# Performance work log

Hardware: AMD Instinct MI355X
Metric: run time of the kernel (lower is better)

The kernel has to match this reference:

```python
import jax, jax.numpy as jnp
import numpy as np

D_MODEL = 1024
EXPAND = 2
D_INNER = D_MODEL * EXPAND
KERNEL = 4
EPS = 1e-5


def setup_inputs() -> dict:
    key = jax.random.key(0)
    ks = jax.random.split(key, 8)
    B, L = 2, 4096
    x = jax.random.normal(ks[0], (B, L, D_MODEL), dtype=jnp.float32)
    norm_w = jnp.ones((D_MODEL,), jnp.float32)
    norm_b = jnp.zeros((D_MODEL,), jnp.float32)
    # torch Linear weight layout [out, in]
    in_proj_w = jax.random.normal(ks[1], (2 * D_INNER, D_MODEL), jnp.float32) / np.sqrt(D_MODEL)
    # depthwise Conv1d weight [d_inner, 1, K]
    conv_w = jax.random.normal(ks[2], (D_INNER, 1, KERNEL), jnp.float32) / np.sqrt(KERNEL)
    conv_b = jax.random.normal(ks[3], (D_INNER,), jnp.float32) * 0.02
    gate_w = jax.random.normal(ks[4], (D_INNER, D_INNER), jnp.float32) / np.sqrt(D_INNER)
    gate_b = jnp.zeros((D_INNER,), jnp.float32)
    out_proj_w = jax.random.normal(ks[5], (D_MODEL, D_INNER), jnp.float32) / np.sqrt(D_INNER)
    return {"x": x, "norm_w": norm_w, "norm_b": norm_b, "in_proj_w": in_proj_w,
            "conv_w": conv_w, "conv_b": conv_b, "gate_w": gate_w, "gate_b": gate_b,
            "out_proj_w": out_proj_w}


def _layernorm(x, w, b):
    mu = jnp.mean(x, axis=-1, keepdims=True)
    var = jnp.var(x, axis=-1, keepdims=True)
    return (x - mu) * jax.lax.rsqrt(var + EPS) * w + b


def _glru(x, norm_w, norm_b, in_proj_w, conv_w, conv_b, gate_w, gate_b, out_proj_w):
    B, L, D = x.shape
    residual = x
    xn = _layernorm(x, norm_w, norm_b)
    xz = jnp.einsum('bld,ed->ble', xn, in_proj_w)  # [B,L,2*d_inner]
    x_inner, z = jnp.split(xz, 2, axis=-1)
    # causal depthwise conv: torch pads 3 both sides then slices [:L] == left-pad 3
    lhs = jnp.transpose(x_inner, (0, 2, 1))  # [B, C, L]
    conv = jax.lax.conv_general_dilated(
        lhs, conv_w, window_strides=(1,), padding=[(KERNEL - 1, 0)],
        feature_group_count=D_INNER,
        dimension_numbers=('NCH', 'OIH', 'NCH'))
    x_conv = jnp.transpose(conv, (0, 2, 1)) + conv_b  # [B, L, C]
    x_conv = jax.nn.silu(x_conv)
    a = jax.nn.sigmoid(jnp.einsum('blc,ec->ble', x_conv, gate_w) + gate_b)
    b = (1.0 - a) * x_conv
    # h_t = a_t * h_{t-1} + b_t, h_0 prior = 0 -> parallel associative scan
    def combine(e1, e2):
        a1, b1 = e1
        a2, b2 = e2
        return a1 * a2, a2 * b1 + b2
    _, y = jax.lax.associative_scan(combine, (a, b), axis=1)
    y = y * jax.nn.silu(z)
    return residual + jnp.einsum('blc,dc->bld', y, out_proj_w)


def reference(x, norm_w, norm_b, in_proj_w, conv_w, conv_b, gate_w, gate_b, out_proj_w):
    return _glru(x, norm_w, norm_b, in_proj_w, conv_w, conv_b, gate_w, gate_b, out_proj_w)
```

## Files before the change

### kernel.cpp

```cpp
#include <hip/hip_runtime.h>
#include <cstdint>

#define D_MODEL 1024
#define D_INNER 2048
#define LSEQ    4096
#define BATCH   2
#define M_ROWS  (BATCH * LSEQ)
#define CHUNK   128
#define NCHUNK  (LSEQ / CHUNK)

typedef unsigned short u16;
typedef __bf16 bf16x8 __attribute__((ext_vector_type(8)));
typedef float f32x4 __attribute__((ext_vector_type(4)));
typedef u16 u16x4 __attribute__((ext_vector_type(4)));

__device__ __forceinline__ u16 f2bf(float f) {
  union { float f; unsigned u; } x; x.f = f;
  unsigned u = x.u;
  unsigned r = (u + 0x7FFFu + ((u >> 16) & 1u)) >> 16;
  return (u16)r;
}
__device__ __forceinline__ float bf2f(u16 h) {
  union { unsigned u; float f; } x; x.u = ((unsigned)h) << 16;
  return x.f;
}
__device__ __forceinline__ float sigmoidf_(float v) { return 1.0f / (1.0f + expf(-v)); }
__device__ __forceinline__ float siluf_(float v)    { return v / (1.0f + expf(-v)); }

__device__ __forceinline__ void gl_lds16(const void* g, void* l) {
  __builtin_amdgcn_global_load_lds(
      (const __attribute__((address_space(1))) void*)g,
      (__attribute__((address_space(3))) void*)l, 16, 0, 0);
}

#define SBAR()   asm volatile("s_barrier" ::: "memory")
#define WAITV0() asm volatile("s_waitcnt vmcnt(0)" ::: "memory")
#define WAITV2() asm volatile("s_waitcnt vmcnt(2)" ::: "memory")
#define WAITV8() asm volatile("s_waitcnt vmcnt(8)" ::: "memory")
#define WAITL0() do { asm volatile("s_waitcnt lgkmcnt(0)" ::: "memory"); __builtin_amdgcn_sched_barrier(0); } while (0)

__global__ void __launch_bounds__(256)
cast_bf16_kernel(const float* __restrict__ in, u16* __restrict__ out, int n4) {
  int i = blockIdx.x * 256 + threadIdx.x;
  if (i < n4) {
    float4 v = ((const float4*)in)[i];
    u16x4 o;
    o.x = f2bf(v.x); o.y = f2bf(v.y); o.z = f2bf(v.z); o.w = f2bf(v.w);
    ((u16x4*)out)[i] = o;
  }
}

__global__ void __launch_bounds__(256)
ln_kernel(const float* __restrict__ x, const float* __restrict__ w,
          const float* __restrict__ b, u16* __restrict__ xn) {
  const int row = blockIdx.x;
  const int t = threadIdx.x;
  const float4 v = ((const float4*)(x + (size_t)row * D_MODEL))[t];
  float s  = v.x + v.y + v.z + v.w;
  float ss = v.x * v.x + v.y * v.y + v.z * v.z + v.w * v.w;
#pragma unroll
  for (int o = 32; o > 0; o >>= 1) {
    s  += __shfl_xor(s, o);
    ss += __shfl_xor(ss, o);
  }
  __shared__ float red[8];
  const int wid = t >> 6, lane = t & 63;
  if (lane == 0) { red[wid] = s; red[4 + wid] = ss; }
  __syncthreads();
  s  = red[0] + red[1] + red[2] + red[3];
  ss = red[4] + red[5] + red[6] + red[7];
  const float mu  = s * (1.0f / D_MODEL);
  const float var = ss * (1.0f / D_MODEL) - mu * mu;
  const float rs  = rsqrtf(var + 1e-5f);
  const float4 wv = ((const float4*)w)[t];
  const float4 bv = ((const float4*)b)[t];
  u16x4 o4;
  o4.x = f2bf((v.x - mu) * rs * wv.x + bv.x);
  o4.y = f2bf((v.y - mu) * rs * wv.y + bv.y);
  o4.z = f2bf((v.z - mu) * rs * wv.z + bv.z);
  o4.w = f2bf((v.w - mu) * rs * wv.w + bv.w);
  ((u16x4*)(xn + (size_t)row * D_MODEL))[t] = o4;
}

#define MFMA_BF16 __builtin_amdgcn_mfma_f32_16x16x32_bf16

template<int EPI>
__global__ void __launch_bounds__(512, 2)
gemm256(const u16* __restrict__ A, const u16* __restrict__ Bm,
        int M, int N, int K,
        const float* __restrict__ ef, float* __restrict__ of,
        u16* __restrict__ ob0, u16* __restrict__ ob1) {
  __shared__ __align__(1024) char lds[131072];
  const int tid  = threadIdx.x;
  const int wid  = tid >> 6, lane = tid & 63;
  const int nbx  = N >> 8;
  const int nwg  = nbx * (M >> 8);
  const int bid  = blockIdx.x;
  const int cpx  = nwg >> 3;
  const int swz  = (bid & 7) * cpx + (bid >> 3);
  const int bx   = swz % nbx, by = swz / nbx;
  const size_t m0 = (size_t)by << 8, n0 = (size_t)bx << 8;

  const int wr = wid >> 2, wc = wid & 3;
  const size_t rb = (size_t)K * 2;
  const size_t rj = (size_t)64 * rb;

  const int srow  = lane >> 3;
  const int sslot = ((lane & 7) ^ srow) << 4;
  const char* gA = (const char*)A  + (m0 + (size_t)(wid * 8 + srow)) * rb + sslot;
  const char* gB = (const char*)Bm + (n0 + (size_t)(wid * 8 + srow)) * rb + sslot;
  const int sdst = wid * 1024;

  const int q    = lane >> 4;
  const int r15  = lane & 15;
  const int cswz0 = (q * 16)      ^ ((lane & 7) << 4);
  const int cswz1 = (64 + q * 16) ^ ((lane & 7) << 4);
  const int paoff = (wr * 128 + r15) * 128;
  const int pboff = (wc * 64  + r15) * 128;

  f32x4 acc[8][4] = {};
  const int nk = K >> 6;

  {
    const char* a = gA; const char* b = gB;
#pragma unroll
    for (int i = 0; i < 4; ++i) {
      gl_lds16(a, lds + sdst + i * 8192);
      gl_lds16(b, lds + 65536 + sdst + i * 8192);
      a += rj; b += rj;
    }
  }
  WAITV0();
  SBAR();

  size_t kb = 128;
  for (int t = 0; t < nk; ++t) {
    const int cur = t & 1;
    const char* At = lds + cur * 32768;
    const char* Bt = lds + 65536 + cur * 32768;
    char* An = lds + (cur ^ 1) * 32768;
    char* Bn = lds + 65536 + (cur ^ 1) * 32768;
    const bool pf = (t + 1 < nk);

    bf16x8 af[4][2], b0[2][2], b1[2][2];

    if (pf) {
      gl_lds16(gA + kb,          An + sdst);
      gl_lds16(gA + kb + 2 * rj, An + sdst + 16384);
      gl_lds16(gB + kb,          Bn + sdst);
      gl_lds16(gB + kb + rj,     Bn + sdst + 8192);
      gl_lds16(gB + kb + 2 * rj, Bn + sdst + 16384);
      gl_lds16(gB + kb + 3 * rj, Bn + sdst + 24576);
      gl_lds16(gA + kb + rj,     An + sdst + 8192);
      gl_lds16(gA + kb + 3 * rj, An + sdst + 24576);
    }
#pragma unroll
    for (int mi = 0; mi < 4; ++mi) {
      af[mi][0] = *(const bf16x8*)(At + paoff + mi * 2048 + cswz0);
      af[mi][1] = *(const bf16x8*)(At + paoff + mi * 2048 + cswz1);
    }
#pragma unroll
    for (int ni = 0; ni < 2; ++ni) {
      b0[ni][0] = *(const bf16x8*)(Bt + pboff + ni * 2048 + cswz0);
      b0[ni][1] = *(const bf16x8*)(Bt + pboff + ni * 2048 + cswz1);
    }
    SBAR();
    WAITL0();
    __builtin_amdgcn_s_setprio(1);
#pragma unroll
    for (int mi = 0; mi < 4; ++mi)
#pragma unroll
      for (int ni = 0; ni < 2; ++ni) {
        acc[mi][ni] = MFMA_BF16(af[mi][0], b0[ni][0], acc[mi][ni], 0, 0, 0);
        acc[mi][ni] = MFMA_BF16(af[mi][1], b0[ni][1], acc[mi][ni], 0, 0, 0);
      }
    __builtin_amdgcn_s_setprio(0);
    SBAR();

#pragma unroll
    for (int ni = 0; ni < 2; ++ni) {
      b1[ni][0] = *(const bf16x8*)(Bt + pboff + (ni + 2) * 2048 + cswz0);
      b1[ni][1] = *(const bf16x8*)(Bt + pboff + (ni + 2) * 2048 + cswz1);
    }
    SBAR();
    WAITL0();
    __builtin_amdgcn_s_setprio(1);
#pragma unroll
    for (int mi = 0; mi < 4; ++mi)
#pragma unroll
      for (int ni = 0; ni < 2; ++ni) {
        acc[mi][ni + 2] = MFMA_BF16(af[mi][0], b1[ni][0], acc[mi][ni + 2], 0, 0, 0);
        acc[mi][ni + 2] = MFMA_BF16(af[mi][1], b1[ni][1], acc[mi][ni + 2], 0, 0, 0);
      }
    __builtin_amdgcn_s_setprio(0);
    if (pf) { WAITV8(); } else { WAITV0(); }
    SBAR();

#pragma unroll
    for (int mi = 0; mi < 4; ++mi) {
      af[mi][0] = *(const bf16x8*)(At + paoff + (mi + 4) * 2048 + cswz0);
      af[mi][1] = *(const bf16x8*)(At + paoff + (mi + 4) * 2048 + cswz1);
    }
    SBAR();
    WAITL0();
    __builtin_amdgcn_s_setprio(1);
#pragma unroll
    for (int mi = 0; mi < 4; ++mi)
#pragma unroll
      for (int ni = 0; ni < 2; ++ni) {
        acc[mi + 4][ni] = MFMA_BF16(af[mi][0], b0[ni][0], acc[mi + 4][ni], 0, 0, 0);
        acc[mi + 4][ni] = MFMA_BF16(af[mi][1], b0[ni][1], acc[mi + 4][ni], 0, 0, 0);
      }
    __builtin_amdgcn_s_setprio(0);
    SBAR();

    __builtin_amdgcn_s_setprio(1);
#pragma unroll
    for (int mi = 0; mi < 4; ++mi)
#pragma unroll
      for (int ni = 0; ni < 2; ++ni) {
        acc[mi + 4][ni + 2] = MFMA_BF16(af[mi][0], b1[ni][0], acc[mi + 4][ni + 2], 0, 0, 0);
        acc[mi + 4][ni + 2] = MFMA_BF16(af[mi][1], b1[ni][1], acc[mi + 4][ni + 2], 0, 0, 0);
      }
    __builtin_amdgcn_s_setprio(0);
    if (pf) { WAITV2(); }
    SBAR();
    kb += 128;
  }

  const int c0 = lane & 15;
  const int r0 = (lane >> 4) << 2;
#pragma unroll
  for (int mi = 0; mi < 8; ++mi) {
#pragma unroll
    for (int ni = 0; ni < 4; ++ni) {
#pragma unroll
      for (int rg = 0; rg < 4; ++rg) {
        const size_t row = m0 + (size_t)(wr * 128 + mi * 16 + r0 + rg);
        const size_t col = n0 + (size_t)(wc * 64 + ni * 16 + c0);
        const float v = acc[mi][ni][rg];
        if (EPI == 0) {
          if (col < (size_t)D_INNER) ob0[row * D_INNER + col] = f2bf(v);
          else                       ob1[row * D_INNER + (col - D_INNER)] = f2bf(siluf_(v));
        } else if (EPI == 1) {
          ob0[row * (size_t)N + col] = f2bf(v);
        } else {
          of[row * (size_t)N + col] = v + ef[row * (size_t)N + col];
        }
      }
    }
  }
}

__global__ void __launch_bounds__(256)
conv_silu_kernel(const u16* __restrict__ xin, const float* __restrict__ cw,
                 const float* __restrict__ cb, u16* __restrict__ xc) {
  const int c   = blockIdx.x * 256 + threadIdx.x;
  const int l0  = blockIdx.y * 8;
  const int bat = blockIdx.z;
  const size_t base = ((size_t)bat * LSEQ) * D_INNER + c;
  const float w0 = cw[c * 4 + 0], w1 = cw[c * 4 + 1], w2 = cw[c * 4 + 2], w3 = cw[c * 4 + 3];
  const float bb = cb[c];
  float v[11];
#pragma unroll
  for (int i = 0; i < 11; ++i) {
    const int l = l0 - 3 + i;
    v[i] = (l >= 0) ? bf2f(xin[base + (size_t)l * D_INNER]) : 0.0f;
  }
#pragma unroll
  for (int r = 0; r < 8; ++r) {
    const float acc = bb + w0 * v[r] + w1 * v[r + 1] + w2 * v[r + 2] + w3 * v[r + 3];
    xc[base + (size_t)(l0 + r) * D_INNER] = f2bf(siluf_(acc));
  }
}

__global__ void __launch_bounds__(256)
scan_a_kernel(const u16* __restrict__ g, const u16* __restrict__ xc,
              const float* __restrict__ gbias,
              float* __restrict__ cA, float* __restrict__ cB) {
  const int c   = (blockIdx.x * 256 + threadIdx.x) * 2;
  const int ch  = blockIdx.y;
  const int bat = blockIdx.z;
  const float bb0 = gbias[c], bb1 = gbias[c + 1];
  size_t idx = ((size_t)bat * LSEQ + (size_t)ch * CHUNK) * D_INNER + c;
  float pA0 = 1.0f, hB0 = 0.0f, pA1 = 1.0f, hB1 = 0.0f;
  for (int t = 0; t < CHUNK; ++t) {
    const ushort2 gg = *(const ushort2*)(g + idx);
    const ushort2 xx = *(const ushort2*)(xc + idx);
    const float a0 = sigmoidf_(bf2f(gg.x) + bb0);
    const float a1 = sigmoidf_(bf2f(gg.y) + bb1);
    pA0 *= a0; hB0 = a0 * hB0 + (1.0f - a0) * bf2f(xx.x);
    pA1 *= a1; hB1 = a1 * hB1 + (1.0f - a1) * bf2f(xx.y);
    idx += D_INNER;
  }
  const size_t o = ((size_t)bat * NCHUNK + ch) * D_INNER + c;
  *(float2*)(cA + o) = make_float2(pA0, pA1);
  *(float2*)(cB + o) = make_float2(hB0, hB1);
}

__global__ void __launch_bounds__(256)
scan_b_kernel(const float* __restrict__ cA, const float* __restrict__ cB,
              float* __restrict__ carry) {
  const int tid = blockIdx.x * 256 + threadIdx.x;
  const int bat = tid >> 11;
  const int c   = tid & (D_INNER - 1);
  float h = 0.0f;
  const size_t base = (size_t)bat * NCHUNK * D_INNER + c;
  for (int i = 0; i < NCHUNK; ++i) {
    const size_t o = base + (size_t)i * D_INNER;
    carry[o] = h;
    h = cA[o] * h + cB[o];
  }
}

__global__ void __launch_bounds__(256)
scan_c_kernel(const u16* __restrict__ g, const u16* __restrict__ xc,
              const u16* __restrict__ sz, const float* __restrict__ gbias,
              const float* __restrict__ carry, u16* __restrict__ yg) {
  const int c   = (blockIdx.x * 256 + threadIdx.x) * 2;
  const int ch  = blockIdx.y;
  const int bat = blockIdx.z;
  const float bb0 = gbias[c], bb1 = gbias[c + 1];
  const float2 h2 = *(const float2*)(carry + ((size_t)bat * NCHUNK + ch) * D_INNER + c);
  float h0 = h2.x, h1 = h2.y;
  size_t idx = ((size_t)bat * LSEQ + (size_t)ch * CHUNK) * D_INNER + c;
  for (int t = 0; t < CHUNK; ++t) {
    const ushort2 gg = *(const ushort2*)(g + idx);
    const ushort2 xx = *(const ushort2*)(xc + idx);
    const ushort2 zz = *(const ushort2*)(sz + idx);
    const float a0 = sigmoidf_(bf2f(gg.x) + bb0);
    const float a1 = sigmoidf_(bf2f(gg.y) + bb1);
    h0 = a0 * h0 + (1.0f - a0) * bf2f(xx.x);
    h1 = a1 * h1 + (1.0f - a1) * bf2f(xx.y);
    ushort2 o2;
    o2.x = f2bf(h0 * bf2f(zz.x));
    o2.y = f2bf(h1 * bf2f(zz.y));
    *(ushort2*)(yg + idx) = o2;
    idx += D_INNER;
  }
}

extern "C" void kernel_launch(void* const* d_in, const int* in_sizes, int n_in,
                              void* d_out, int out_size, void* d_ws, size_t ws_size,
                              hipStream_t stream) {
  const float* x         = (const float*)d_in[0];
  const float* norm_w    = (const float*)d_in[1];
  const float* norm_b    = (const float*)d_in[2];
  const float* in_proj_w = (const float*)d_in[3];
  const float* conv_w    = (const float*)d_in[4];
  const float* conv_b    = (const float*)d_in[5];
  const float* gate_w    = (const float*)d_in[6];
  const float* gate_b    = (const float*)d_in[7];
  const float* out_proj_w= (const float*)d_in[8];
  float* out = (float*)d_out;

  char* p = (char*)d_ws;
  u16* xn      = (u16*)p; p += (size_t)M_ROWS * D_MODEL * 2;
  u16* w_in    = (u16*)p; p += (size_t)2 * D_INNER * D_MODEL * 2;
  u16* w_gate  = (u16*)p; p += (size_t)D_INNER * D_INNER * 2;
  u16* w_out   = (u16*)p; p += (size_t)D_MODEL * D_INNER * 2;
  u16* x_inner = (u16*)p; p += (size_t)M_ROWS * D_INNER * 2;
  u16* szb     = (u16*)p; p += (size_t)M_ROWS * D_INNER * 2;
  u16* xconv   = (u16*)p; p += (size_t)M_ROWS * D_INNER * 2;
  u16* gbuf    = (u16*)p; p += (size_t)M_ROWS * D_INNER * 2;
  u16* yg      = (u16*)p; p += (size_t)M_ROWS * D_INNER * 2;
  float* cA    = (float*)p; p += (size_t)BATCH * NCHUNK * D_INNER * 4;
  float* cB    = (float*)p; p += (size_t)BATCH * NCHUNK * D_INNER * 4;
  float* carry = (float*)p; p += (size_t)BATCH * NCHUNK * D_INNER * 4;
  if ((size_t)(p - (char*)d_ws) > ws_size) return;

  cast_bf16_kernel<<<dim3(2 * D_INNER * D_MODEL / 4 / 256), 256, 0, stream>>>(in_proj_w, w_in, 2 * D_INNER * D_MODEL / 4);
  cast_bf16_kernel<<<dim3(D_INNER * D_INNER / 4 / 256), 256, 0, stream>>>(gate_w, w_gate, D_INNER * D_INNER / 4);
  cast_bf16_kernel<<<dim3(D_MODEL * D_INNER / 4 / 256), 256, 0, stream>>>(out_proj_w, w_out, D_MODEL * D_INNER / 4);

  ln_kernel<<<dim3(M_ROWS), 256, 0, stream>>>(x, norm_w, norm_b, xn);

  gemm256<0><<<dim3((M_ROWS / 256) * (2 * D_INNER / 256)), 512, 0, stream>>>(
      xn, w_in, M_ROWS, 2 * D_INNER, D_MODEL, nullptr, nullptr, x_inner, szb);

  conv_silu_kernel<<<dim3(D_INNER / 256, LSEQ / 8, BATCH), 256, 0, stream>>>(x_inner, conv_w, conv_b, xconv);

  gemm256<1><<<dim3((M_ROWS / 256) * (D_INNER / 256)), 512, 0, stream>>>(
      xconv, w_gate, M_ROWS, D_INNER, D_INNER, nullptr, nullptr, gbuf, nullptr);

  scan_a_kernel<<<dim3(D_INNER / 512, NCHUNK, BATCH), 256, 0, stream>>>(gbuf, xconv, gate_b, cA, cB);
  scan_b_kernel<<<dim3(BATCH * D_INNER / 256), 256, 0, stream>>>(cA, cB, carry);
  scan_c_kernel<<<dim3(D_INNER / 512, NCHUNK, BATCH), 256, 0, stream>>>(gbuf, xconv, szb, gate_b, carry, yg);

  gemm256<2><<<dim3((M_ROWS / 256) * (D_MODEL / 256)), 512, 0, stream>>>(
      yg, w_out, M_ROWS, D_MODEL, D_INNER, x, out, nullptr, nullptr);
}
```

Measured before the change: 368.0 us.

## Software-pipeline GEMM LDS fragment loads across k-iterations and drop occupancy hint

Restructures the gemm256 main loop so the A-low and B0 fragments for the next k-tile are read from LDS at the end of the current iteration, overlapping LDS reads with MFMA work. Several barriers and explicit lgkmcnt waits are removed, and the global-to-LDS prefetch is split into two phases with new vmcnt wait points. The launch-bounds occupancy hint of 2 blocks is dropped, giving the compiler more registers for the extra live fragments at the cost of possible occupancy. The epilogue branch on column is hoisted to a per-block flag.

```diff
diff --git a/kernel.cpp b/kernel.cpp
--- a/kernel.cpp
+++ b/kernel.cpp
@@ -35,9 +35,7 @@
 
 #define SBAR()   asm volatile("s_barrier" ::: "memory")
 #define WAITV0() asm volatile("s_waitcnt vmcnt(0)" ::: "memory")
-#define WAITV2() asm volatile("s_waitcnt vmcnt(2)" ::: "memory")
-#define WAITV8() asm volatile("s_waitcnt vmcnt(8)" ::: "memory")
-#define WAITL0() do { asm volatile("s_waitcnt lgkmcnt(0)" ::: "memory"); __builtin_amdgcn_sched_barrier(0); } while (0)
+#define WAITV6() asm volatile("s_waitcnt vmcnt(6)" ::: "memory")
 
 __global__ void __launch_bounds__(256)
 cast_bf16_kernel(const float* __restrict__ in, u16* __restrict__ out, int n4) {
@@ -85,7 +83,7 @@
 #define MFMA_BF16 __builtin_amdgcn_mfma_f32_16x16x32_bf16
 
 template<int EPI>
-__global__ void __launch_bounds__(512, 2)
+__global__ void __launch_bounds__(512)
 gemm256(const u16* __restrict__ A, const u16* __restrict__ Bm,
         int M, int N, int K,
         const float* __restrict__ ef, float* __restrict__ of,
@@ -119,6 +117,7 @@
   const int pboff = (wc * 64  + r15) * 128;
 
   f32x4 acc[8][4] = {};
+  bf16x8 afL[4][2], afH[4][2], b0r[2][2], b1r[2][2];
   const int nk = K >> 6;
 
   {
@@ -132,6 +131,20 @@
   }
   WAITV0();
   SBAR();
+  {
+    const char* At = lds;
+    const char* Bt = lds + 65536;
+#pragma unroll
+    for (int mi = 0; mi < 4; ++mi) {
+      afL[mi][0] = *(const bf16x8*)(At + paoff + mi * 2048 + cswz0);
+      afL[mi][1] = *(const bf16x8*)(At + paoff + mi * 2048 + cswz1);
+    }
+#pragma unroll
+    for (int ni = 0; ni < 2; ++ni) {
+      b0r[ni][0] = *(const bf16x8*)(Bt + pboff + ni * 2048 + cswz0);
+      b0r[ni][1] = *(const bf16x8*)(Bt + pboff + ni * 2048 + cswz1);
+    }
+  }
 
   size_t kb = 128;
   for (int t = 0; t < nk; ++t) {
@@ -142,8 +155,6 @@
     char* Bn = lds + 65536 + (cur ^ 1) * 32768;
     const bool pf = (t + 1 < nk);
 
-    bf16x8 af[4][2], b0[2][2], b1[2][2];
-
     if (pf) {
       gl_lds16(gA + kb,          An + sdst);
       gl_lds16(gA + kb + 2 * rj, An + sdst + 16384);
@@ -151,85 +162,82 @@
       gl_lds16(gB + kb + rj,     Bn + sdst + 8192);
       gl_lds16(gB + kb + 2 * rj, Bn + sdst + 16384);
       gl_lds16(gB + kb + 3 * rj, Bn + sdst + 24576);
+    }
+#pragma unroll
+    for (int ni = 0; ni < 2; ++ni) {
+      b1r[ni][0] = *(const bf16x8*)(Bt + pboff + (ni + 2) * 2048 + cswz0);
+      b1r[ni][1] = *(const bf16x8*)(Bt + pboff + (ni + 2) * 2048 + cswz1);
+    }
+    __builtin_amdgcn_s_setprio(1);
+#pragma unroll
+    for (int mi = 0; mi < 4; ++mi)
+#pragma unroll
+      for (int ni = 0; ni < 2; ++ni) {
+        acc[mi][ni] = MFMA_BF16(afL[mi][0], b0r[ni][0], acc[mi][ni], 0, 0, 0);
+        acc[mi][ni] = MFMA_BF16(afL[mi][1], b0r[ni][1], acc[mi][ni], 0, 0, 0);
+      }
+    __builtin_amdgcn_s_setprio(0);
+    if (pf) { WAITV6(); } else { WAITV0(); }
+    SBAR();
+
+#pragma unroll
+    for (int mi = 0; mi < 4; ++mi) {
+      afH[mi][0] = *(const bf16x8*)(At + paoff + (mi + 4) * 2048 + cswz0);
+      afH[mi][1] = *(const bf16x8*)(At + paoff + (mi + 4) * 2048 + cswz1);
+    }
+    __builtin_amdgcn_s_setprio(1);
+#pragma unroll
+    for (int mi = 0; mi < 4; ++mi)
+#pragma unroll
+      for (int ni = 0; ni < 2; ++ni) {
+        acc[mi][ni + 2] = MFMA_BF16(afL[mi][0], b1r[ni][0], acc[mi][ni + 2], 0, 0, 0);
+        acc[mi][ni + 2] = MFMA_BF16(afL[mi][1], b1r[ni][1], acc[mi][ni + 2], 0, 0, 0);
+      }
+    __builtin_amdgcn_s_setprio(0);
+    SBAR();
+
+    __builtin_amdgcn_s_setprio(1);
+#pragma unroll
+    for (int mi = 0; mi < 4; ++mi)
+#pragma unroll
+      for (int ni = 0; ni < 2; ++ni) {
+        acc[mi + 4][ni] = MFMA_BF16(afH[mi][0], b0r[ni][0], acc[mi + 4][ni], 0, 0, 0);
+        acc[mi + 4][ni] = MFMA_BF16(afH[mi][1], b0r[ni][1], acc[mi + 4][ni], 0, 0, 0);
+      }
+    __builtin_amdgcn_s_setprio(0);
+    WAITV0();
+    SBAR();
+
+    if (pf) {
       gl_lds16(gA + kb + rj,     An + sdst + 8192);
       gl_lds16(gA + kb + 3 * rj, An + sdst + 24576);
-    }
-#pragma unroll
-    for (int mi = 0; mi < 4; ++mi) {
-      af[mi][0] = *(const bf16x8*)(At + paoff + mi * 2048 + cswz0);
-      af[mi][1] = *(const bf16x8*)(At + paoff + mi * 2048 + cswz1);
-    }
-#pragma unroll
-    for (int ni = 0; ni < 2; ++ni) {
-      b0[ni][0] = *(const bf16x8*)(Bt + pboff + ni * 2048 + cswz0);
-      b0[ni][1] = *(const bf16x8*)(Bt + pboff + ni * 2048 + cswz1);
-    }
-    SBAR();
-    WAITL0();
+#pragma unroll
+      for (int mi = 0; mi < 4; ++mi) {
+        afL[mi][0] = *(const bf16x8*)(An + paoff + mi * 2048 + cswz0);
+        afL[mi][1] = *(const bf16x8*)(An + paoff + mi * 2048 + cswz1);
+      }
+#pragma unroll
+      for (int ni = 0; ni < 2; ++ni) {
+        b0r[ni][0] = *(const bf16x8*)(Bn + pboff + ni * 2048 + cswz0);
+        b0r[ni][1] = *(const bf16x8*)(Bn + pboff + ni * 2048 + cswz1);
+      }
+    }
     __builtin_amdgcn_s_setprio(1);
 #pragma unroll
     for (int mi = 0; mi < 4; ++mi)
 #pragma unroll
       for (int ni = 0; ni < 2; ++ni) {
-        acc[mi][ni] = MFMA_BF16(af[mi][0], b0[ni][0], acc[mi][ni], 0, 0, 0);
-        acc[mi][ni] = MFMA_BF16(af[mi][1], b0[ni][1], acc[mi][ni], 0, 0, 0);
+        acc[mi + 4][ni + 2] = MFMA_BF16(afH[mi][0], b1r[ni][0], acc[mi + 4][ni + 2], 0, 0, 0);
+        acc[mi + 4][ni + 2] = MFMA_BF16(afH[mi][1], b1r[ni][1], acc[mi + 4][ni + 2], 0, 0, 0);
       }
     __builtin_amdgcn_s_setprio(0);
     SBAR();
-
-#pragma unroll
-    for (int ni = 0; ni < 2; ++ni) {
-      b1[ni][0] = *(const bf16x8*)(Bt + pboff + (ni + 2) * 2048 + cswz0);
-      b1[ni][1] = *(const bf16x8*)(Bt + pboff + (ni + 2) * 2048 + cswz1);
-    }
-    SBAR();
-    WAITL0();
-    __builtin_amdgcn_s_setprio(1);
-#pragma unroll
-    for (int mi = 0; mi < 4; ++mi)
-#pragma unroll
-      for (int ni = 0; ni < 2; ++ni) {
-        acc[mi][ni + 2] = MFMA_BF16(af[mi][0], b1[ni][0], acc[mi][ni + 2], 0, 0, 0);
-        acc[mi][ni + 2] = MFMA_BF16(af[mi][1], b1[ni][1], acc[mi][ni + 2], 0, 0, 0);
-      }
-    __builtin_amdgcn_s_setprio(0);
-    if (pf) { WAITV8(); } else { WAITV0(); }
-    SBAR();
-
-#pragma unroll
-    for (int mi = 0; mi < 4; ++mi) {
-      af[mi][0] = *(const bf16x8*)(At + paoff + (mi + 4) * 2048 + cswz0);
-      af[mi][1] = *(const bf16x8*)(At + paoff + (mi + 4) * 2048 + cswz1);
-    }
-    SBAR();
-    WAITL0();
-    __builtin_amdgcn_s_setprio(1);
-#pragma unroll
-    for (int mi = 0; mi < 4; ++mi)
-#pragma unroll
-      for (int ni = 0; ni < 2; ++ni) {
-        acc[mi + 4][ni] = MFMA_BF16(af[mi][0], b0[ni][0], acc[mi + 4][ni], 0, 0, 0);
-        acc[mi + 4][ni] = MFMA_BF16(af[mi][1], b0[ni][1], acc[mi + 4][ni], 0, 0, 0);
-      }
-    __builtin_amdgcn_s_setprio(0);
-    SBAR();
-
-    __builtin_amdgcn_s_setprio(1);
-#pragma unroll
-    for (int mi = 0; mi < 4; ++mi)
-#pragma unroll
-      for (int ni = 0; ni < 2; ++ni) {
-        acc[mi + 4][ni + 2] = MFMA_BF16(af[mi][0], b1[ni][0], acc[mi + 4][ni + 2], 0, 0, 0);
-        acc[mi + 4][ni + 2] = MFMA_BF16(af[mi][1], b1[ni][1], acc[mi + 4][ni + 2], 0, 0, 0);
-      }
-    __builtin_amdgcn_s_setprio(0);
-    if (pf) { WAITV2(); }
-    SBAR();
     kb += 128;
   }
 
   const int c0 = lane & 15;
   const int r0 = (lane >> 4) << 2;
+  const bool isz = (EPI == 0) && (n0 >= (size_t)D_INNER);
 #pragma unroll
   for (int mi = 0; mi < 8; ++mi) {
 #pragma unroll
@@ -240,8 +248,8 @@
         const size_t col = n0 + (size_t)(wc * 64 + ni * 16 + c0);
         const float v = acc[mi][ni][rg];
         if (EPI == 0) {
-          if (col < (size_t)D_INNER) ob0[row * D_INNER + col] = f2bf(v);
-          else                       ob1[row * D_INNER + (col - D_INNER)] = f2bf(siluf_(v));
+          if (!isz) ob0[row * D_INNER + col] = f2bf(v);
+          else      ob1[row * D_INNER + (col - D_INNER)] = f2bf(siluf_(v));
         } else if (EPI == 1) {
           ob0[row * (size_t)N + col] = f2bf(v);
         } else {
```

Measured after the change: 348.8 us. 1.05x faster.
